# Optimization experiments

Measured on AMD Instinct MI355X. Metric: run time of the kernel, lower is better.

## Reference

```python
import jax, jax.numpy as jnp
import numpy as np

EPS = 1e-06

def rms_norm(x, g, eps=EPS):
    # normalize over last (channel) dim, then scale
    return x * jax.lax.rsqrt(jnp.mean(x * x, axis=-1, keepdims=True) + eps) * g

def apply_rope(x, theta):
    # x: [B,S,N,D]; theta: [S,1,D//2] angles; equivalent to complex mult by exp(i*theta)
    cos = jnp.cos(theta)[None]  # [1,S,1,D//2]
    sin = jnp.sin(theta)[None]
    x1 = x[..., 0::2]
    x2 = x[..., 1::2]
    r = x1 * cos - x2 * sin
    i = x1 * sin + x2 * cos
    return jnp.stack([r, i], axis=-1).reshape(x.shape)

def setup_inputs() -> dict:
    key = jax.random.key(0)
    ks = jax.random.split(key, 16)
    B, L, C, N, D, S = 1, 1024, 2048, 16, 128, 8192
    std = 0.02
    inp = {
        "x": jax.random.normal(ks[0], (B, L, C), jnp.float32),
        "cache_k": jax.random.normal(ks[1], (B, S, N, D), jnp.float32),
        "cache_v": jax.random.normal(ks[2], (B, S, N, D), jnp.float32),
        "write_indices": jnp.arange(L, dtype=jnp.int32),
        "attn_mask": jnp.ones((1, 1, 1, S), bool),
        "rope_theta": jax.random.uniform(ks[3], (L, 1, D // 2), jnp.float32) * (2.0 * np.pi),
        "Wq": jax.random.normal(ks[4], (C, C), jnp.float32) * std,
        "bq": jnp.zeros((C,), jnp.float32),
        "Wk": jax.random.normal(ks[5], (C, C), jnp.float32) * std,
        "bk": jnp.zeros((C,), jnp.float32),
        "Wv": jax.random.normal(ks[6], (C, C), jnp.float32) * std,
        "bv": jnp.zeros((C,), jnp.float32),
        "Wo": jax.random.normal(ks[7], (C, C), jnp.float32) * std,
        "bo": jnp.zeros((C,), jnp.float32),
        "gq": jnp.ones((C,), jnp.float32),
        "gk": jnp.ones((C,), jnp.float32),
    }
    return inp

def reference(x, cache_k, cache_v, write_indices, attn_mask, rope_theta,
              Wq, bq, Wk, bk, Wv, bv, Wo, bo, gq, gk):
    B, L, C = x.shape
    N, D = cache_k.shape[2], cache_k.shape[3]
    q = rms_norm(x @ Wq + bq, gq).reshape(B, L, N, D)
    k = rms_norm(x @ Wk + bk, gk).reshape(B, L, N, D)
    v = (x @ Wv + bv).reshape(B, L, N, D)
    q = apply_rope(q, rope_theta)
    k = apply_rope(k, rope_theta)
    # ring-buffer cache write
    ck = cache_k.at[:, write_indices].set(k)
    cv = cache_v.at[:, write_indices].set(v)
    # attention against full cache
    scale = 1.0 / jnp.sqrt(jnp.asarray(D, x.dtype))
    scores = jnp.einsum('blnd,bsnd->bnls', q, ck) * scale  # [B,N,L,S]
    scores = jnp.where(attn_mask, scores, jnp.asarray(-1e30, scores.dtype))
    attn = jax.nn.softmax(scores, axis=-1)
    out = jnp.einsum('bnls,bsnd->blnd', attn, cv).reshape(B, L, C)
    return out @ Wo + bo
```

## Files before the change

kernel.cpp:

```cpp
#include <hip/hip_runtime.h>

typedef __bf16 bf16;
typedef bf16 bf16x8 __attribute__((ext_vector_type(8)));
typedef bf16 bf16x4 __attribute__((ext_vector_type(4)));
typedef float f32x4 __attribute__((ext_vector_type(4)));
typedef float f32x16 __attribute__((ext_vector_type(16)));

#define MFMA16(a, b, c) __builtin_amdgcn_mfma_f32_16x16x32_bf16(a, b, c, 0, 0, 0)
#define MFMA32(a, b, c) __builtin_amdgcn_mfma_f32_32x32x16_bf16(a, b, c, 0, 0, 0)

__device__ __forceinline__ void async16(const bf16* g, bf16* l) {
    __builtin_amdgcn_global_load_lds(
        (const __attribute__((address_space(1))) unsigned int*)(g),
        (__attribute__((address_space(3))) unsigned int*)(l), 16, 0, 0);
}

__device__ __forceinline__ unsigned int pkbf(float a, float b) {
    union { bf16 h[2]; unsigned int u; } x;
    x.h[0] = (bf16)a; x.h[1] = (bf16)b;
    return x.u;
}

__global__ __launch_bounds__(256) void k_prep(
    const float* __restrict__ x, bf16* __restrict__ xbf,
    const float* __restrict__ Wq, const float* __restrict__ Wk,
    const float* __restrict__ Wv, const float* __restrict__ Wo,
    bf16* __restrict__ WqT, bf16* __restrict__ WkT,
    bf16* __restrict__ WvT, bf16* __restrict__ WoT) {
    __shared__ bf16 lt[64][72];
    int b = blockIdx.x, t = threadIdx.x;
    if (b < 1024) {
        int i = (b * 256 + t) * 8;
        const float4* p = (const float4*)(x + i);
        float4 a = p[0], c = p[1];
        bf16x8 v;
        v[0] = (bf16)a.x; v[1] = (bf16)a.y; v[2] = (bf16)a.z; v[3] = (bf16)a.w;
        v[4] = (bf16)c.x; v[5] = (bf16)c.y; v[6] = (bf16)c.z; v[7] = (bf16)c.w;
        *(bf16x8*)(xbf + i) = v;
        return;
    }
    int wb = b - 1024;
    int wid = wb >> 10, rem = wb & 1023;
    const float* W = wid == 0 ? Wq : (wid == 1 ? Wk : (wid == 2 ? Wv : Wo));
    bf16* WT = wid == 0 ? WqT : (wid == 1 ? WkT : (wid == 2 ? WvT : WoT));
    int n0 = (rem & 31) * 64, k0 = (rem >> 5) * 64;
#pragma unroll
    for (int j = 0; j < 4; j++) {
        int idx = t + 256 * j;
        int r = idx >> 4;
        int c4 = (idx & 15) << 2;
        float4 v = *(const float4*)&W[(size_t)(k0 + r) * 2048 + n0 + c4];
        lt[r][c4] = (bf16)v.x; lt[r][c4 + 1] = (bf16)v.y;
        lt[r][c4 + 2] = (bf16)v.z; lt[r][c4 + 3] = (bf16)v.w;
    }
    __syncthreads();
#pragma unroll
    for (int j = 0; j < 4; j++) {
        int idx = t + 256 * j;
        int n = idx >> 4;
        int k4 = (idx & 15) << 2;
        bf16x4 o;
        o[0] = lt[k4][n]; o[1] = lt[k4 + 1][n]; o[2] = lt[k4 + 2][n]; o[3] = lt[k4 + 3][n];
        *(bf16x4*)&WT[(size_t)(n0 + n) * 2048 + k0 + k4] = o;
    }
}

__global__ __launch_bounds__(256) void k_gemm(
    const bf16* __restrict__ A,
    const bf16* __restrict__ B0, const bf16* __restrict__ B1, const bf16* __restrict__ B2,
    const float* __restrict__ c0, const float* __restrict__ c1, const float* __restrict__ c2,
    float* __restrict__ D0, float* __restrict__ D1, float* __restrict__ D2) {
    const int N = 2048, K = 2048;
    const bf16* Bt = blockIdx.z == 0 ? B0 : (blockIdx.z == 1 ? B1 : B2);
    const float* bias = blockIdx.z == 0 ? c0 : (blockIdx.z == 1 ? c1 : c2);
    float* D = blockIdx.z == 0 ? D0 : (blockIdx.z == 1 ? D1 : D2);
    __shared__ bf16 Al[64 * 32];
    __shared__ bf16 Bl[128 * 32];
    int t = threadIdx.x;
    int lane = t & 63, w = t >> 6;
    int l15 = lane & 15, g = lane >> 4;
    int wr = w >> 1, wc = w & 1;
    int m0 = blockIdx.y * 64, n0 = blockIdx.x * 128;
    f32x4 acc[2][4] = {};
    int arow = t >> 2, acol = (t & 3) * 8;
    for (int k0 = 0; k0 < K; k0 += 32) {
        async16(&A[(size_t)(m0 + arow) * K + k0 + acol], Al + t * 8);
        async16(&Bt[(size_t)(n0 + arow) * K + k0 + acol], Bl + t * 8);
        async16(&Bt[(size_t)(n0 + 64 + arow) * K + k0 + acol], Bl + 2048 + t * 8);
        __syncthreads();
        bf16x8 af[2], bfr[4];
#pragma unroll
        for (int i = 0; i < 2; i++) af[i] = *(const bf16x8*)&Al[(wr * 32 + i * 16 + l15) * 32 + g * 8];
#pragma unroll
        for (int i = 0; i < 4; i++) bfr[i] = *(const bf16x8*)&Bl[(wc * 64 + i * 16 + l15) * 32 + g * 8];
#pragma unroll
        for (int mi = 0; mi < 2; mi++)
#pragma unroll
            for (int ni = 0; ni < 4; ni++)
                acc[mi][ni] = MFMA16(af[mi], bfr[ni], acc[mi][ni]);
        __syncthreads();
    }
#pragma unroll
    for (int mi = 0; mi < 2; mi++) {
#pragma unroll
        for (int ni = 0; ni < 4; ni++) {
            int n = n0 + wc * 64 + ni * 16 + l15;
            float bv = bias[n];
#pragma unroll
            for (int r = 0; r < 4; r++) {
                int m = m0 + wr * 32 + mi * 16 + g * 4 + r;
                D[(size_t)m * N + n] = acc[mi][ni][r] + bv;
            }
        }
    }
}

__global__ __launch_bounds__(256) void k_post(
    const float* __restrict__ qraw, const float* __restrict__ kraw, const float* __restrict__ vraw,
    const float* __restrict__ cache_k, const float* __restrict__ cache_v,
    const float* __restrict__ gq, const float* __restrict__ gk,
    const float* __restrict__ theta,
    bf16* __restrict__ Qb, bf16* __restrict__ Kb, bf16* __restrict__ Vt) {
    __shared__ bf16 lt[64][132];
    __shared__ float rq[4], rk[4];
    int b = blockIdx.x, t = threadIdx.x;
    if (b < 1024) {
        int l = b;
        int lane = t & 63, w = t >> 6;
        int c = t * 8;
        float qv[8], kv[8];
        const float4* qp = (const float4*)(qraw + (size_t)l * 2048 + c);
        const float4* kp = (const float4*)(kraw + (size_t)l * 2048 + c);
        float4 a;
        a = qp[0]; qv[0] = a.x; qv[1] = a.y; qv[2] = a.z; qv[3] = a.w;
        a = qp[1]; qv[4] = a.x; qv[5] = a.y; qv[6] = a.z; qv[7] = a.w;
        a = kp[0]; kv[0] = a.x; kv[1] = a.y; kv[2] = a.z; kv[3] = a.w;
        a = kp[1]; kv[4] = a.x; kv[5] = a.y; kv[6] = a.z; kv[7] = a.w;
        float ssq = 0.f, ssk = 0.f;
#pragma unroll
        for (int j = 0; j < 8; j++) { ssq += qv[j] * qv[j]; ssk += kv[j] * kv[j]; }
#pragma unroll
        for (int m = 1; m < 64; m <<= 1) { ssq += __shfl_xor(ssq, m); ssk += __shfl_xor(ssk, m); }
        if (lane == 0) { rq[w] = ssq; rk[w] = ssk; }
        __syncthreads();
        ssq = rq[0] + rq[1] + rq[2] + rq[3];
        ssk = rk[0] + rk[1] + rk[2] + rk[3];
        float iq = rsqrtf(ssq * (1.0f / 2048.0f) + 1e-6f);
        float ik = rsqrtf(ssk * (1.0f / 2048.0f) + 1e-6f);
#pragma unroll
        for (int j = 0; j < 8; j++) { qv[j] *= iq * gq[c + j]; kv[j] *= ik * gk[c + j]; }
        int h = c >> 7, dd = c & 127;
        bf16x8 qo, ko;
        const float SC = 1.4426950408889634f / 11.313708498984761f;
#pragma unroll
        for (int p = 0; p < 4; p++) {
            float th = theta[l * 64 + (dd >> 1) + p];
            float sn, cs;
            __sincosf(th, &sn, &cs);
            float qr = qv[2 * p] * cs - qv[2 * p + 1] * sn;
            float qi = qv[2 * p] * sn + qv[2 * p + 1] * cs;
            float kr = kv[2 * p] * cs - kv[2 * p + 1] * sn;
            float ki = kv[2 * p] * sn + kv[2 * p + 1] * cs;
            qo[2 * p] = (bf16)(qr * SC); qo[2 * p + 1] = (bf16)(qi * SC);
            ko[2 * p] = (bf16)kr;        ko[2 * p + 1] = (bf16)ki;
        }
        *(bf16x8*)&Qb[(size_t)h * 131072 + (size_t)l * 128 + dd] = qo;
        *(bf16x8*)&Kb[(size_t)h * 1048576 + (size_t)l * 128 + dd] = ko;
        return;
    }
    if (b < 3072) {
        int vb = b - 1024;
        int st = vb & 127, n = vb >> 7;
        int s0 = st * 64;
        const float* src = (s0 < 1024) ? (vraw + (size_t)s0 * 2048) : (cache_v + (size_t)s0 * 2048);
#pragma unroll
        for (int j = 0; j < 8; j++) {
            int idx = t + 256 * j;
            int i = idx >> 5;
            int d4 = (idx & 31) << 2;
            float4 v = *(const float4*)&src[(size_t)i * 2048 + n * 128 + d4];
            lt[i][d4] = (bf16)v.x; lt[i][d4 + 1] = (bf16)v.y;
            lt[i][d4 + 2] = (bf16)v.z; lt[i][d4 + 3] = (bf16)v.w;
        }
        __syncthreads();
        int d = t >> 1, sh = (t & 1) << 5;
        bf16* dst = Vt + (size_t)n * 1048576 + (size_t)d * 8192 + s0 + sh;
#pragma unroll
        for (int q = 0; q < 4; q++) {
            bf16x8 o;
#pragma unroll
            for (int e = 0; e < 8; e++) o[e] = lt[sh + q * 8 + e][d];
            *(bf16x8*)&dst[q * 8] = o;
        }
        return;
    }
    int s = 1024 + (b - 3072);
    int e = t * 8;
    int n = e >> 7, d = e & 127;
    const float4* p = (const float4*)&cache_k[(size_t)s * 2048 + e];
    float4 a = p[0], c2 = p[1];
    bf16x8 v;
    v[0] = (bf16)a.x; v[1] = (bf16)a.y; v[2] = (bf16)a.z; v[3] = (bf16)a.w;
    v[4] = (bf16)c2.x; v[5] = (bf16)c2.y; v[6] = (bf16)c2.z; v[7] = (bf16)c2.w;
    *(bf16x8*)&Kb[(size_t)n * 1048576 + (size_t)s * 128 + d] = v;
}

__global__ __launch_bounds__(256, 2) void k_flash(
    const bf16* __restrict__ Qb, const bf16* __restrict__ Kb, const bf16* __restrict__ Vt,
    float* __restrict__ Opart, float2* __restrict__ MLpart) {
    int b = blockIdx.x;
    int cx = b & 7, jj = b >> 3;
    int p = cx + 8 * (jj >> 3);
    int qb = jj & 7;
    int h = p & 15, z = p >> 4;
    int q0 = qb * 128;
    int t = threadIdx.x;
    int lane = t & 63, wq = t >> 6;
    int l31 = lane & 31, hi = lane >> 5;
    __shared__ bf16 Kl[64 * 128];
    __shared__ bf16 Vl[128 * 64];
    const bf16* Kh = Kb + (size_t)h * 1048576;
    const bf16* Vh = Vt + (size_t)h * 1048576;
    int q = q0 + wq * 32 + l31;
    bf16x8 qf[8];
#pragma unroll
    for (int db = 0; db < 8; db++)
        qf[db] = *(const bf16x8*)&Qb[(size_t)h * 131072 + (size_t)q * 128 + db * 16 + hi * 8];
    f32x16 o[4] = {};
    float mm = -1e30f, ll = 0.f;
    int krow = t >> 4;
    int kcol = (t & 15) * 8;
    int kdst = krow * 128 + (((t & 15) ^ (krow & 7)) * 8);
    int vrow = t >> 3;
    int vcol = (t & 7) * 8;
    int vdst = vrow * 64 + (((t & 7) ^ (vrow & 7)) * 8);
    int swr = (l31 & 7) << 3;
    int it0 = z * 32, it1 = it0 + 32;
    bf16x8 kst[4], vst[4];
    {
        int s0 = it0 * 64;
#pragma unroll
        for (int j = 0; j < 4; j++)
            kst[j] = *(const bf16x8*)&Kh[(size_t)(s0 + krow + 16 * j) * 128 + kcol];
#pragma unroll
        for (int j = 0; j < 4; j++)
            vst[j] = *(const bf16x8*)&Vh[(size_t)(vrow + 32 * j) * 8192 + s0 + vcol];
    }
    for (int it = it0; it < it1; ++it) {
        __syncthreads();
#pragma unroll
        for (int j = 0; j < 4; j++) *(bf16x8*)&Kl[kdst + j * 2048] = kst[j];
#pragma unroll
        for (int j = 0; j < 4; j++) *(bf16x8*)&Vl[vdst + j * 2048] = vst[j];
        __syncthreads();
        if (it + 1 < it1) {
            int s1 = (it + 1) * 64;
#pragma unroll
            for (int j = 0; j < 4; j++)
                kst[j] = *(const bf16x8*)&Kh[(size_t)(s1 + krow + 16 * j) * 128 + kcol];
#pragma unroll
            for (int j = 0; j < 4; j++)
                vst[j] = *(const bf16x8*)&Vh[(size_t)(vrow + 32 * j) * 8192 + s1 + vcol];
        }
        f32x16 sA = {}, sB = {};
        __builtin_amdgcn_s_setprio(1);
#pragma unroll
        for (int db = 0; db < 8; db++) {
            int doff = (db * 16 + hi * 8) ^ swr;
            bf16x8 ka = *(const bf16x8*)&Kl[l31 * 128 + doff];
            bf16x8 kb = *(const bf16x8*)&Kl[(32 + l31) * 128 + doff];
            sA = MFMA32(ka, qf[db], sA);
            sB = MFMA32(kb, qf[db], sB);
        }
        __builtin_amdgcn_s_setprio(0);
        float tm = -1e30f;
#pragma unroll
        for (int r = 0; r < 16; r++) { tm = fmaxf(tm, sA[r]); tm = fmaxf(tm, sB[r]); }
        tm = fmaxf(tm, __shfl_xor(tm, 32));
        if (__any(tm > mm + 11.5416f)) {
            float mn = fmaxf(mm, tm);
            float al = exp2f(mm - mn);
#pragma unroll
            for (int dt = 0; dt < 4; dt++)
#pragma unroll
                for (int r = 0; r < 16; r++) o[dt][r] *= al;
            ll *= al; mm = mn;
        }
        float ps = 0.f;
#pragma unroll
        for (int r = 0; r < 16; r++) { sA[r] = exp2f(sA[r] - mm); ps += sA[r]; }
#pragma unroll
        for (int r = 0; r < 16; r++) { sB[r] = exp2f(sB[r] - mm); ps += sB[r]; }
        ll += ps + __shfl_xor(ps, 32);
        unsigned int w0[8], w1[8];
#pragma unroll
        for (int qd = 0; qd < 4; qd++) {
            w0[qd * 2]     = pkbf(sA[qd * 4], sA[qd * 4 + 1]);
            w0[qd * 2 + 1] = pkbf(sA[qd * 4 + 2], sA[qd * 4 + 3]);
            w1[qd * 2]     = pkbf(sB[qd * 4], sB[qd * 4 + 1]);
            w1[qd * 2 + 1] = pkbf(sB[qd * 4 + 2], sB[qd * 4 + 3]);
        }
#pragma unroll
        for (int ks = 0; ks < 4; ks++) {
            const int a4 = (ks & 1) * 4;
            unsigned int oo0, oo1, ss0, ss1;
            if ((ks >> 1) == 0) {
                oo0 = hi ? w0[a4 + 2] : w0[a4];
                oo1 = hi ? w0[a4 + 3] : w0[a4 + 1];
                ss0 = hi ? w0[a4] : w0[a4 + 2];
                ss1 = hi ? w0[a4 + 1] : w0[a4 + 3];
            } else {
                oo0 = hi ? w1[a4 + 2] : w1[a4];
                oo1 = hi ? w1[a4 + 3] : w1[a4 + 1];
                ss0 = hi ? w1[a4] : w1[a4 + 2];
                ss1 = hi ? w1[a4 + 1] : w1[a4 + 3];
            }
            unsigned int x0 = (unsigned int)__shfl_xor((int)ss0, 32);
            unsigned int x1 = (unsigned int)__shfl_xor((int)ss1, 32);
            union { unsigned int w[4]; bf16x8 v; } fr;
            fr.w[0] = hi ? x0 : oo0;
            fr.w[1] = hi ? x1 : oo1;
            fr.w[2] = hi ? oo0 : x0;
            fr.w[3] = hi ? oo1 : x1;
            __builtin_amdgcn_s_setprio(1);
#pragma unroll
            for (int dt = 0; dt < 4; dt++) {
                int e = (dt * 32 + l31) * 64 + ((ks * 16 + hi * 8) ^ swr);
                bf16x8 vf = *(const bf16x8*)&Vl[e];
                o[dt] = MFMA32(vf, fr.v, o[dt]);
            }
            __builtin_amdgcn_s_setprio(0);
        }
    }
    size_t obase = ((size_t)(z * 16 + h) * 1024 + q) * 128 + hi * 64;
#pragma unroll
    for (int dt = 0; dt < 4; dt++) {
#pragma unroll
        for (int c = 0; c < 4; c++) {
            float4 f = make_float4(o[dt][4 * c], o[dt][4 * c + 1],
                                   o[dt][4 * c + 2], o[dt][4 * c + 3]);
            *(float4*)&Opart[obase + dt * 16 + c * 4] = f;
        }
    }
    if (hi == 0) MLpart[(size_t)(z * 16 + h) * 1024 + q] = make_float2(mm, ll);
}

__global__ __launch_bounds__(256) void k_combine(
    const float* __restrict__ Opart, const float2* __restrict__ MLpart,
    bf16* __restrict__ Ob) {
    int q = blockIdx.x, t = threadIdx.x;
    int h = t >> 4, pb = (t & 15) * 8;
    int hi = pb >> 6, dt = (pb >> 4) & 3, c = (pb >> 2) & 3;
    int da = dt * 32 + 8 * c + 4 * hi;
    int db = dt * 32 + 8 * (c + 1) + 4 * hi;
    float m[4], l[4];
#pragma unroll
    for (int z = 0; z < 4; z++) {
        float2 v = MLpart[(size_t)(z * 16 + h) * 1024 + q];
        m[z] = v.x; l[z] = v.y;
    }
    float M = -1e30f;
#pragma unroll
    for (int z = 0; z < 4; z++) M = fmaxf(M, m[z]);
    float e[4], den = 0.f;
#pragma unroll
    for (int z = 0; z < 4; z++) { e[z] = exp2f(m[z] - M); den += e[z] * l[z]; }
    float inv = 1.0f / den;
    float acc[8] = {};
#pragma unroll
    for (int z = 0; z < 4; z++) {
        const float4* p = (const float4*)&Opart[((size_t)(z * 16 + h) * 1024 + q) * 128 + pb];
        float4 a = p[0], b2 = p[1];
        float s = e[z] * inv;
        acc[0] += a.x * s; acc[1] += a.y * s; acc[2] += a.z * s; acc[3] += a.w * s;
        acc[4] += b2.x * s; acc[5] += b2.y * s; acc[6] += b2.z * s; acc[7] += b2.w * s;
    }
    bf16x4 oa, ob;
#pragma unroll
    for (int j = 0; j < 4; j++) { oa[j] = (bf16)acc[j]; ob[j] = (bf16)acc[4 + j]; }
    *(bf16x4*)&Ob[(size_t)q * 2048 + h * 128 + da] = oa;
    *(bf16x4*)&Ob[(size_t)q * 2048 + h * 128 + db] = ob;
}

extern "C" void kernel_launch(void* const* d_in, const int* in_sizes, int n_in,
                              void* d_out, int out_size, void* d_ws, size_t ws_size,
                              hipStream_t stream) {
    const float* x       = (const float*)d_in[0];
    const float* cache_k = (const float*)d_in[1];
    const float* cache_v = (const float*)d_in[2];
    const float* theta   = (const float*)d_in[5];
    const float* Wq = (const float*)d_in[6];
    const float* bq = (const float*)d_in[7];
    const float* Wk = (const float*)d_in[8];
    const float* bk = (const float*)d_in[9];
    const float* Wv = (const float*)d_in[10];
    const float* bv = (const float*)d_in[11];
    const float* Wo = (const float*)d_in[12];
    const float* bo = (const float*)d_in[13];
    const float* gq = (const float*)d_in[14];
    const float* gk = (const float*)d_in[15];
    float* out = (float*)d_out;

    bf16* xbf = (bf16*)d_ws;
    bf16* WoT = xbf + 2097152;
    bf16* WqT = WoT + 4194304;
    bf16* WkT = WqT + 4194304;
    bf16* WvT = WkT + 4194304;
    float* qraw = (float*)(WvT + 4194304);
    float* kraw = qraw + 2097152;
    float* vraw = kraw + 2097152;
    bf16* Qb = (bf16*)(vraw + 2097152);
    bf16* Kb = Qb + 2097152;
    bf16* Vt = Kb + 16777216;
    bf16* Ob = Vt + 16777216;

    float* Opart = (float*)WqT;
    float2* MLpart = (float2*)xbf;

    k_prep<<<5120, 256, 0, stream>>>(x, xbf, Wq, Wk, Wv, Wo, WqT, WkT, WvT, WoT);
    k_gemm<<<dim3(16, 16, 3), 256, 0, stream>>>(xbf, WqT, WkT, WvT, bq, bk, bv, qraw, kraw, vraw);
    k_post<<<10240, 256, 0, stream>>>(qraw, kraw, vraw, cache_k, cache_v, gq, gk, theta, Qb, Kb, Vt);
    k_flash<<<512, 256, 0, stream>>>(Qb, Kb, Vt, Opart, MLpart);
    k_combine<<<1024, 256, 0, stream>>>(Opart, MLpart, Ob);
    k_gemm<<<dim3(16, 16, 1), 256, 0, stream>>>(Ob, WoT, WoT, WoT, bo, bo, bo, out, out, out);
}
```

Baseline: 242.0 us.

## Split attention KV range six ways, use async LDS loads, retile output GEMM

The flash kernel now splits the 8192-key range into six chunks instead of four, launching 768 blocks with a three-blocks-per-CU occupancy hint. The combine kernel merges six partial results to match. K/V tiles now go straight from global memory into LDS through global_load_lds, with the XOR swizzle moved to the source address. This replaces the register staging and software prefetch and lowers register pressure, at the cost of an extra barrier per iteration and less overlap between loading and compute. The bf16 packing of P is now done per k-step, and the output projection GEMM uses a 32-row M tile, doubling its block count for better CU fill.

```diff
diff --git a/kernel.cpp b/kernel.cpp
--- a/kernel.cpp
+++ b/kernel.cpp
@@ -65,50 +65,52 @@
     }
 }
 
+template <int MT>
 __global__ __launch_bounds__(256) void k_gemm(
     const bf16* __restrict__ A,
     const bf16* __restrict__ B0, const bf16* __restrict__ B1, const bf16* __restrict__ B2,
     const float* __restrict__ c0, const float* __restrict__ c1, const float* __restrict__ c2,
     float* __restrict__ D0, float* __restrict__ D1, float* __restrict__ D2) {
     const int N = 2048, K = 2048;
+    const int WROWS = MT / 2, MI = WROWS / 16;
     const bf16* Bt = blockIdx.z == 0 ? B0 : (blockIdx.z == 1 ? B1 : B2);
     const float* bias = blockIdx.z == 0 ? c0 : (blockIdx.z == 1 ? c1 : c2);
     float* D = blockIdx.z == 0 ? D0 : (blockIdx.z == 1 ? D1 : D2);
-    __shared__ bf16 Al[64 * 32];
+    __shared__ bf16 Al[MT * 32];
     __shared__ bf16 Bl[128 * 32];
     int t = threadIdx.x;
     int lane = t & 63, w = t >> 6;
     int l15 = lane & 15, g = lane >> 4;
     int wr = w >> 1, wc = w & 1;
-    int m0 = blockIdx.y * 64, n0 = blockIdx.x * 128;
-    f32x4 acc[2][4] = {};
+    int m0 = blockIdx.y * MT, n0 = blockIdx.x * 128;
+    f32x4 acc[MI][4] = {};
     int arow = t >> 2, acol = (t & 3) * 8;
     for (int k0 = 0; k0 < K; k0 += 32) {
-        async16(&A[(size_t)(m0 + arow) * K + k0 + acol], Al + t * 8);
+        if (t < MT * 4) async16(&A[(size_t)(m0 + arow) * K + k0 + acol], Al + t * 8);
         async16(&Bt[(size_t)(n0 + arow) * K + k0 + acol], Bl + t * 8);
         async16(&Bt[(size_t)(n0 + 64 + arow) * K + k0 + acol], Bl + 2048 + t * 8);
         __syncthreads();
-        bf16x8 af[2], bfr[4];
-#pragma unroll
-        for (int i = 0; i < 2; i++) af[i] = *(const bf16x8*)&Al[(wr * 32 + i * 16 + l15) * 32 + g * 8];
+        bf16x8 af[MI], bfr[4];
+#pragma unroll
+        for (int i = 0; i < MI; i++) af[i] = *(const bf16x8*)&Al[(wr * WROWS + i * 16 + l15) * 32 + g * 8];
 #pragma unroll
         for (int i = 0; i < 4; i++) bfr[i] = *(const bf16x8*)&Bl[(wc * 64 + i * 16 + l15) * 32 + g * 8];
 #pragma unroll
-        for (int mi = 0; mi < 2; mi++)
+        for (int mi = 0; mi < MI; mi++)
 #pragma unroll
             for (int ni = 0; ni < 4; ni++)
                 acc[mi][ni] = MFMA16(af[mi], bfr[ni], acc[mi][ni]);
         __syncthreads();
     }
 #pragma unroll
-    for (int mi = 0; mi < 2; mi++) {
+    for (int mi = 0; mi < MI; mi++) {
 #pragma unroll
         for (int ni = 0; ni < 4; ni++) {
             int n = n0 + wc * 64 + ni * 16 + l15;
             float bv = bias[n];
 #pragma unroll
             for (int r = 0; r < 4; r++) {
-                int m = m0 + wr * 32 + mi * 16 + g * 4 + r;
+                int m = m0 + wr * WROWS + mi * 16 + g * 4 + r;
                 D[(size_t)m * N + n] = acc[mi][ni][r] + bv;
             }
         }
@@ -205,7 +207,7 @@
     *(bf16x8*)&Kb[(size_t)n * 1048576 + (size_t)s * 128 + d] = v;
 }
 
-__global__ __launch_bounds__(256, 2) void k_flash(
+__global__ __launch_bounds__(256, 3) void k_flash(
     const bf16* __restrict__ Qb, const bf16* __restrict__ Kb, const bf16* __restrict__ Vt,
     float* __restrict__ Opart, float2* __restrict__ MLpart) {
     int b = blockIdx.x;
@@ -229,39 +231,22 @@
     f32x16 o[4] = {};
     float mm = -1e30f, ll = 0.f;
     int krow = t >> 4;
-    int kcol = (t & 15) * 8;
-    int kdst = krow * 128 + (((t & 15) ^ (krow & 7)) * 8);
+    int kcs = ((t & 15) ^ (krow & 7)) * 8;
     int vrow = t >> 3;
-    int vcol = (t & 7) * 8;
-    int vdst = vrow * 64 + (((t & 7) ^ (vrow & 7)) * 8);
+    int vcs = ((t & 7) ^ (vrow & 7)) * 8;
+    bf16* Kld = (bf16*)Kl + t * 8;
+    bf16* Vld = (bf16*)Vl + t * 8;
     int swr = (l31 & 7) << 3;
-    int it0 = z * 32, it1 = it0 + 32;
-    bf16x8 kst[4], vst[4];
-    {
-        int s0 = it0 * 64;
+    int it0 = (128 * z) / 6, it1 = (128 * (z + 1)) / 6;
+    for (int it = it0; it < it1; ++it) {
+        int s0 = it * 64;
 #pragma unroll
         for (int j = 0; j < 4; j++)
-            kst[j] = *(const bf16x8*)&Kh[(size_t)(s0 + krow + 16 * j) * 128 + kcol];
+            async16(&Kh[(size_t)(s0 + krow + 16 * j) * 128 + kcs], Kld + 2048 * j);
 #pragma unroll
         for (int j = 0; j < 4; j++)
-            vst[j] = *(const bf16x8*)&Vh[(size_t)(vrow + 32 * j) * 8192 + s0 + vcol];
-    }
-    for (int it = it0; it < it1; ++it) {
-        __syncthreads();
-#pragma unroll
-        for (int j = 0; j < 4; j++) *(bf16x8*)&Kl[kdst + j * 2048] = kst[j];
-#pragma unroll
-        for (int j = 0; j < 4; j++) *(bf16x8*)&Vl[vdst + j * 2048] = vst[j];
-        __syncthreads();
-        if (it + 1 < it1) {
-            int s1 = (it + 1) * 64;
-#pragma unroll
-            for (int j = 0; j < 4; j++)
-                kst[j] = *(const bf16x8*)&Kh[(size_t)(s1 + krow + 16 * j) * 128 + kcol];
-#pragma unroll
-            for (int j = 0; j < 4; j++)
-                vst[j] = *(const bf16x8*)&Vh[(size_t)(vrow + 32 * j) * 8192 + s1 + vcol];
-        }
+            async16(&Vh[(size_t)(vrow + 32 * j) * 8192 + s0 + vcs], Vld + 2048 * j);
+        __syncthreads();
         f32x16 sA = {}, sB = {};
         __builtin_amdgcn_s_setprio(1);
 #pragma unroll
@@ -292,29 +277,23 @@
 #pragma unroll
         for (int r = 0; r < 16; r++) { sB[r] = exp2f(sB[r] - mm); ps += sB[r]; }
         ll += ps + __shfl_xor(ps, 32);
-        unsigned int w0[8], w1[8];
-#pragma unroll
-        for (int qd = 0; qd < 4; qd++) {
-            w0[qd * 2]     = pkbf(sA[qd * 4], sA[qd * 4 + 1]);
-            w0[qd * 2 + 1] = pkbf(sA[qd * 4 + 2], sA[qd * 4 + 3]);
-            w1[qd * 2]     = pkbf(sB[qd * 4], sB[qd * 4 + 1]);
-            w1[qd * 2 + 1] = pkbf(sB[qd * 4 + 2], sB[qd * 4 + 3]);
-        }
 #pragma unroll
         for (int ks = 0; ks < 4; ks++) {
             const int a4 = (ks & 1) * 4;
-            unsigned int oo0, oo1, ss0, ss1;
-            if ((ks >> 1) == 0) {
-                oo0 = hi ? w0[a4 + 2] : w0[a4];
-                oo1 = hi ? w0[a4 + 3] : w0[a4 + 1];
-                ss0 = hi ? w0[a4] : w0[a4 + 2];
-                ss1 = hi ? w0[a4 + 1] : w0[a4 + 3];
-            } else {
-                oo0 = hi ? w1[a4 + 2] : w1[a4];
-                oo1 = hi ? w1[a4 + 3] : w1[a4 + 1];
-                ss0 = hi ? w1[a4] : w1[a4 + 2];
-                ss1 = hi ? w1[a4 + 1] : w1[a4 + 3];
+            unsigned int wv[4];
+#pragma unroll
+            for (int i = 0; i < 4; i++) {
+                int idx = a4 + i;
+                int qd = idx >> 1, hf = idx & 1;
+                if (ks < 2)
+                    wv[i] = pkbf(sA[qd * 4 + hf * 2], sA[qd * 4 + hf * 2 + 1]);
+                else
+                    wv[i] = pkbf(sB[qd * 4 + hf * 2], sB[qd * 4 + hf * 2 + 1]);
             }
+            unsigned int oo0 = hi ? wv[2] : wv[0];
+            unsigned int oo1 = hi ? wv[3] : wv[1];
+            unsigned int ss0 = hi ? wv[0] : wv[2];
+            unsigned int ss1 = hi ? wv[1] : wv[3];
             unsigned int x0 = (unsigned int)__shfl_xor((int)ss0, 32);
             unsigned int x1 = (unsigned int)__shfl_xor((int)ss1, 32);
             union { unsigned int w[4]; bf16x8 v; } fr;
@@ -331,6 +310,7 @@
             }
             __builtin_amdgcn_s_setprio(0);
         }
+        __syncthreads();
     }
     size_t obase = ((size_t)(z * 16 + h) * 1024 + q) * 128 + hi * 64;
 #pragma unroll
@@ -353,22 +333,22 @@
     int hi = pb >> 6, dt = (pb >> 4) & 3, c = (pb >> 2) & 3;
     int da = dt * 32 + 8 * c + 4 * hi;
     int db = dt * 32 + 8 * (c + 1) + 4 * hi;
-    float m[4], l[4];
-#pragma unroll
-    for (int z = 0; z < 4; z++) {
+    float m[6], l[6];
+#pragma unroll
+    for (int z = 0; z < 6; z++) {
         float2 v = MLpart[(size_t)(z * 16 + h) * 1024 + q];
         m[z] = v.x; l[z] = v.y;
     }
     float M = -1e30f;
 #pragma unroll
-    for (int z = 0; z < 4; z++) M = fmaxf(M, m[z]);
-    float e[4], den = 0.f;
-#pragma unroll
-    for (int z = 0; z < 4; z++) { e[z] = exp2f(m[z] - M); den += e[z] * l[z]; }
+    for (int z = 0; z < 6; z++) M = fmaxf(M, m[z]);
+    float e[6], den = 0.f;
+#pragma unroll
+    for (int z = 0; z < 6; z++) { e[z] = exp2f(m[z] - M); den += e[z] * l[z]; }
     float inv = 1.0f / den;
     float acc[8] = {};
 #pragma unroll
-    for (int z = 0; z < 4; z++) {
+    for (int z = 0; z < 6; z++) {
         const float4* p = (const float4*)&Opart[((size_t)(z * 16 + h) * 1024 + q) * 128 + pb];
         float4 a = p[0], b2 = p[1];
         float s = e[z] * inv;
@@ -418,9 +398,9 @@
     float2* MLpart = (float2*)xbf;
 
     k_prep<<<5120, 256, 0, stream>>>(x, xbf, Wq, Wk, Wv, Wo, WqT, WkT, WvT, WoT);
-    k_gemm<<<dim3(16, 16, 3), 256, 0, stream>>>(xbf, WqT, WkT, WvT, bq, bk, bv, qraw, kraw, vraw);
+    k_gemm<64><<<dim3(16, 16, 3), 256, 0, stream>>>(xbf, WqT, WkT, WvT, bq, bk, bv, qraw, kraw, vraw);
     k_post<<<10240, 256, 0, stream>>>(qraw, kraw, vraw, cache_k, cache_v, gq, gk, theta, Qb, Kb, Vt);
-    k_flash<<<512, 256, 0, stream>>>(Qb, Kb, Vt, Opart, MLpart);
+    k_flash<<<768, 256, 0, stream>>>(Qb, Kb, Vt, Opart, MLpart);
     k_combine<<<1024, 256, 0, stream>>>(Opart, MLpart, Ob);
-    k_gemm<<<dim3(16, 16, 1), 256, 0, stream>>>(Ob, WoT, WoT, WoT, bo, bo, bo, out, out, out);
-}
+    k_gemm<32><<<dim3(16, 32, 1), 256, 0, stream>>>(Ob, WoT, WoT, WoT, bo, bo, bo, out, out, out);
+}
```

After: 246.9 us. 1.02x slower.
